# Kernel tuning notes

Hardware: AMD Instinct MI355X
Metric: run time of the kernel (lower is better)

The kernel has to match this reference:

```python
import jax, jax.numpy as jnp
from jax import lax
import numpy as np


def _bn(x, g, b, eps=1e-5):
    # BatchNorm2d in training mode: biased batch stats over (N,H,W) per channel
    m = jnp.mean(x, axis=(0, 2, 3), keepdims=True)
    v = jnp.mean((x - m) ** 2, axis=(0, 2, 3), keepdims=True)
    return (x - m) * lax.rsqrt(v + eps) * g[None, :, None, None] + b[None, :, None, None]


def _conv(x, w, b, pad):
    y = lax.conv_general_dilated(x, w, (1, 1), [(pad, pad), (pad, pad)],
                                 dimension_numbers=('NCHW', 'OIHW', 'NCHW'))
    return y + b[None, :, None, None]


def _prelu(x, a):
    return jnp.where(x >= 0, x, a * x)


def _maxpool2(x):
    return lax.reduce_window(x, -jnp.inf, lax.max, (1, 1, 2, 2), (1, 1, 2, 2), 'VALID')


def _up2(x):
    # UpsamplingBilinear2d(scale_factor=2) -> bilinear, align_corners=True
    B, C, H, W = x.shape
    def idx(n):
        pos = jnp.arange(2 * n, dtype=x.dtype) * (n - 1) / (2 * n - 1)
        lo = jnp.floor(pos).astype(jnp.int32)
        hi = jnp.minimum(lo + 1, n - 1)
        return lo, hi, pos - lo.astype(x.dtype)
    lo, hi, f = idx(H)
    x = x[:, :, lo, :] * (1 - f)[:, None] + x[:, :, hi, :] * f[:, None]
    lo, hi, f = idx(W)
    x = x[:, :, :, lo] * (1 - f) + x[:, :, :, hi] * f
    return x


def _forward(x, n16, sigma16, bias16, prelu_a,
             bn3_g, bn3_b, bn32_g, bn32_b, bn64_g, bn64_b, bn128_g, bn128_b,
             w1, b1, w2, b2, w3, b3, w4, b4, w5, b5, w6, b6, w7, b7, w11, b11):
    B, C, H, W = x.shape
    # 16 enhancement curves fused: r_k = x^{n_k} / (x^{n_k} + sigma_k^{n_k} + bias_k)
    xn = x[None] ** n16[:, None, None, None, None]          # (16,B,3,H,W)
    r = xn / (xn + (sigma16 ** n16)[:, None, None, None, None]
              + bias16[:, None, None, None, None])
    # each branch gets its own BatchNorm2d(3) stats (same affine params)
    r = jax.vmap(lambda t: _bn(t, bn3_g, bn3_b))(r)
    x_fusion = jnp.transpose(r, (1, 0, 2, 3, 4)).reshape(B, 16 * C, H, W)
    x1 = _bn(_maxpool2(_prelu(_conv(x_fusion, w1, b1, 1), prelu_a)), bn32_g, bn32_b)
    x2 = _bn(_maxpool2(_prelu(_conv(x1, w2, b2, 1), prelu_a)), bn64_g, bn64_b)
    x3 = _bn(_maxpool2(_prelu(_conv(x2, w3, b3, 1), prelu_a)), bn128_g, bn128_b)
    x4 = _bn(_conv(x3, w4, b4, 1), bn128_g, bn128_b)
    x5 = _bn(_up2(_prelu(_conv(jnp.concatenate([x4, x3], 1), w5, b5, 1), prelu_a)), bn64_g, bn64_b)
    x6 = _bn(_up2(_prelu(_conv(jnp.concatenate([x2, x5], 1), w6, b6, 1), prelu_a)), bn32_g, bn32_b)
    x_out = jax.nn.sigmoid(_up2(_prelu(_conv(jnp.concatenate([x1, x6], 1), w7, b7, 1), prelu_a)))
    x_out = _conv(x_out, w11, b11, 0)
    x_mean = jnp.mean(x, axis=1, keepdims=True)
    x_out1 = jnp.mean(x_out, axis=1, keepdims=True)
    return x_out1 * (x / (x_mean + 1e-6))


def setup_inputs() -> dict:
    key = jax.random.key(0)
    ks = jax.random.split(key, 16)
    B, H, W = 8, 256, 256
    nf = 32
    x = jax.random.uniform(ks[0], (B, 3, H, W), jnp.float32, 1e-3, 1.0)
    n16 = jnp.arange(1, 17, dtype=jnp.float32) * 0.5
    sigma16 = jnp.full((16,), 0.5, jnp.float32)
    bias16 = jnp.full((16,), 1e-4, jnp.float32)
    prelu_a = jnp.float32(0.25)
    def cw(k, o, i, kk):
        return jax.random.normal(k, (o, i, kk, kk), jnp.float32) * 0.05
    def cb(o):
        return jnp.zeros((o,), jnp.float32)
    return dict(
        x=x, n16=n16, sigma16=sigma16, bias16=bias16, prelu_a=prelu_a,
        bn3_g=jnp.ones((3,), jnp.float32), bn3_b=jnp.zeros((3,), jnp.float32),
        bn32_g=jnp.ones((32,), jnp.float32), bn32_b=jnp.zeros((32,), jnp.float32),
        bn64_g=jnp.ones((64,), jnp.float32), bn64_b=jnp.zeros((64,), jnp.float32),
        bn128_g=jnp.ones((128,), jnp.float32), bn128_b=jnp.zeros((128,), jnp.float32),
        w1=cw(ks[1], nf, 48, 3), b1=cb(nf),
        w2=cw(ks[2], 2 * nf, nf, 3), b2=cb(2 * nf),
        w3=cw(ks[3], 4 * nf, 2 * nf, 3), b3=cb(4 * nf),
        w4=cw(ks[4], 4 * nf, 4 * nf, 3), b4=cb(4 * nf),
        w5=cw(ks[5], 2 * nf, 8 * nf, 3), b5=cb(2 * nf),
        w6=cw(ks[6], nf, 4 * nf, 3), b6=cb(nf),
        w7=cw(ks[7], nf, 2 * nf, 3), b7=cb(nf),
        w11=cw(ks[8], 3, nf, 1), b11=cb(3),
    )


def reference(x, n16, sigma16, bias16, prelu_a,
              bn3_g, bn3_b, bn32_g, bn32_b, bn64_g, bn64_b, bn128_g, bn128_b,
              w1, b1, w2, b2, w3, b3, w4, b4, w5, b5, w6, b6, w7, b7, w11, b11):
    return _forward(x, n16, sigma16, bias16, prelu_a,
                    bn3_g, bn3_b, bn32_g, bn32_b, bn64_g, bn64_b, bn128_g, bn128_b,
                    w1, b1, w2, b2, w3, b3, w4, b4, w5, b5, w6, b6, w7, b7, w11, b11)
```

## Files before the change

### kernel.cpp

```cpp
#include <hip/hip_runtime.h>

#define FAST_EXP2(x) __builtin_amdgcn_exp2f(x)
#define FAST_LOG2(x) __builtin_amdgcn_logf(x)
#define FAST_RCP(x)  __builtin_amdgcn_rcpf(x)

static constexpr size_t S3_SUM=0,   S3_SQ=48;
static constexpr size_t S32A_SUM=96,  S32A_SQ=128;
static constexpr size_t S64A_SUM=160, S64A_SQ=224;
static constexpr size_t S128A_SUM=288,S128A_SQ=416;
static constexpr size_t S128B_SUM=544,S128B_SQ=672;
static constexpr size_t S64B_SUM=800, S64B_SQ=864;
static constexpr size_t S32B_SUM=928, S32B_SQ=960;
static constexpr size_t A3_=1024,  B3_=1072;
static constexpr size_t A32A_=1120, B32A_=1152;
static constexpr size_t A64A_=1184, B64A_=1248;
static constexpr size_t A128A_=1312,B128A_=1440;
static constexpr size_t A128B_=1568,B128B_=1696;
static constexpr size_t A64B_=1824, B64B_=1888;
static constexpr size_t A32B_=1952, B32B_=1984;
static constexpr size_t SPB_=2016, WBAR_=2032, BBAR_=2064;
static constexpr size_t T1_=4096;
static constexpr size_t T2_=T1_+4194304;
static constexpr size_t T3_=T2_+2097152;
static constexpr size_t T4_=T3_+1048576;
static constexpr size_t C5_=T4_+1048576;
static constexpr size_t U5_=C5_+524288;
static constexpr size_t C6_=U5_+2097152;
static constexpr size_t U6_=C6_+1048576;
static constexpr size_t C7_=U6_+4194304;

__global__ void k_precomp(const float* __restrict__ n16, const float* __restrict__ sig16,
                          const float* __restrict__ b16, const float* __restrict__ w11,
                          const float* __restrict__ b11,
                          float* __restrict__ spb, float* __restrict__ wbar, float* __restrict__ bbar)
{
    int t = threadIdx.x;
    if (t < 16) spb[t] = powf(sig16[t], n16[t]) + b16[t];
    else if (t < 48) { int j = t - 16; wbar[j] = (w11[j] + w11[32 + j] + w11[64 + j]) * (1.f/3.f); }
    else if (t == 48) bbar[0] = (b11[0] + b11[1] + b11[2]) * (1.f/3.f);
}

__global__ __launch_bounds__(256) void k_branch_stats(
    const float* __restrict__ x, const float* __restrict__ n16,
    const float* __restrict__ sig16, const float* __restrict__ b16,
    float* __restrict__ sum, float* __restrict__ sq)
{
    const int c = blockIdx.x >> 6;
    const int chunk = blockIdx.x & 63;
    float nk[16], den[16];
#pragma unroll
    for (int k = 0; k < 16; ++k) { nk[k] = n16[k]; den[k] = powf(sig16[k], nk[k]) + b16[k]; }
    float s[16], q[16];
#pragma unroll
    for (int k = 0; k < 16; ++k) { s[k] = 0.f; q[k] = 0.f; }
    const int per = 8192;
    int start = chunk * per;
    for (int i = start + (int)threadIdx.x; i < start + per; i += 256) {
        int b = i >> 16, hw = i & 65535;
        float xv = x[(size_t)(b*3 + c)*65536 + hw];
        float t = FAST_LOG2(xv);
#pragma unroll
        for (int k = 0; k < 16; ++k) {
            float v = FAST_EXP2(nk[k]*t);
            float r = v * FAST_RCP(v + den[k]);
            s[k] += r; q[k] += r*r;
        }
    }
    __shared__ float red[4][32];
    int lane = threadIdx.x & 63, wid = threadIdx.x >> 6;
#pragma unroll
    for (int k = 0; k < 16; ++k) {
#pragma unroll
        for (int off = 32; off > 0; off >>= 1) {
            s[k] += __shfl_down(s[k], off);
            q[k] += __shfl_down(q[k], off);
        }
    }
    if (lane == 0) {
#pragma unroll
        for (int k = 0; k < 16; ++k) { red[wid][k] = s[k]; red[wid][16+k] = q[k]; }
    }
    __syncthreads();
    if (threadIdx.x < 32) {
        float v = red[0][threadIdx.x] + red[1][threadIdx.x] + red[2][threadIdx.x] + red[3][threadIdx.x];
        int k = threadIdx.x & 15;
        if (threadIdx.x < 16) atomicAdd(&sum[k*3 + c], v);
        else                  atomicAdd(&sq[k*3 + c], v);
    }
}

__global__ __launch_bounds__(256) void k_stats(
    const float* __restrict__ in, int C, int HW, int nchunks, int per,
    float* __restrict__ sum, float* __restrict__ sq)
{
    int c = blockIdx.x / nchunks;
    int chunk = blockIdx.x - c*nchunks;
    float s = 0.f, q = 0.f;
    int start = chunk * per, end = start + per;
    for (int i = start + (int)threadIdx.x; i < end; i += 256) {
        int b = i / HW, hw = i - b*HW;
        float v = in[((size_t)b*C + c)*HW + hw];
        s += v; q += v*v;
    }
#pragma unroll
    for (int off = 32; off > 0; off >>= 1) { s += __shfl_down(s, off); q += __shfl_down(q, off); }
    __shared__ float ss[4], qq[4];
    int lane = threadIdx.x & 63, wid = threadIdx.x >> 6;
    if (lane == 0) { ss[wid] = s; qq[wid] = q; }
    __syncthreads();
    if (threadIdx.x == 0) {
        atomicAdd(&sum[c], ss[0]+ss[1]+ss[2]+ss[3]);
        atomicAdd(&sq[c],  qq[0]+qq[1]+qq[2]+qq[3]);
    }
}

__global__ void k_finalize(const float* __restrict__ sum, const float* __restrict__ sq,
                           const float* __restrict__ g, const float* __restrict__ bb,
                           int C, int gdim, float invN,
                           float* __restrict__ A, float* __restrict__ Bs)
{
    int i = blockIdx.x*blockDim.x + threadIdx.x;
    if (i < C) {
        float m   = sum[i]*invN;
        float var = fmaxf(sq[i]*invN - m*m, 0.f);
        float inv = rsqrtf(var + 1e-5f);
        float a   = g[i % gdim]*inv;
        A[i]  = a;
        Bs[i] = bb[i % gdim] - m*a;
    }
}

__global__ __launch_bounds__(256) void k_fill(
    float* __restrict__ out, const float* __restrict__ bias, int C, int HW, int total)
{
    int idx = blockIdx.x*256 + threadIdx.x;
    if (idx < total) {
        int c = (idx / HW) % C;
        out[idx] = bias[c];
    }
}

template<int COG>
__global__ __launch_bounds__(256,3) void k_conv1f(
    const float* __restrict__ x,
    const float* __restrict__ n16, const float* __restrict__ spb,
    const float* __restrict__ A, const float* __restrict__ Bs,
    const float* __restrict__ w, const float* __restrict__ bias,
    const float* __restrict__ prelu_a,
    float* __restrict__ out)
{
    const int tx = threadIdx.x & 15, ty = threadIdx.x >> 4;
    const int nco = 32 / COG;
    const int b = blockIdx.z / nco, cob = (blockIdx.z - b*nco)*COG;
    const int x0 = blockIdx.x*32, y0 = blockIdx.y*32;

    __shared__ float wl[COG*48*9];
    __shared__ float tl[3*1224];
    __shared__ float rl[3*1224];
    __shared__ float al[48], bl[48], nl[16], dl[16];

    for (int t = threadIdx.x; t < COG*48*9; t += 256) {
        int co = t % COG; int rest = t / COG;
        int kk = rest % 9; int ci = rest / 9;
        wl[t] = w[(((size_t)(cob+co))*48 + ci)*9 + kk];
    }
    if (threadIdx.x < 48) { al[threadIdx.x] = A[threadIdx.x]; bl[threadIdx.x] = Bs[threadIdx.x]; }
    else if (threadIdx.x < 64)  nl[threadIdx.x-48] = n16[threadIdx.x-48];
    else if (threadIdx.x < 80)  dl[threadIdx.x-64] = spb[threadIdx.x-64];

    int off_[14]; int chpack = 0; int okf = 0;
#pragma unroll
    for (int j = 0; j < 14; ++j) {
        int i = threadIdx.x + 256*j;
        if (i < 3468) {
            int ch = i / 1156, jj = i - ch*1156;
            int rr = jj / 34, cc = jj - rr*34;
            int gy = y0 - 1 + rr, gx = x0 - 1 + cc;
            bool ok = (unsigned)gy < 256u && (unsigned)gx < 256u;
            off_[j] = ch*1224 + rr*36 + cc;
            chpack |= ch << (2*j);
            if (ok) {
                okf |= 1 << j;
                tl[off_[j]] = FAST_LOG2(x[((size_t)(b*3+ch))*65536 + gy*256 + gx]);
            } else tl[off_[j]] = 0.f;
        } else off_[j] = 3671;
    }

    float acc[COG][4];
#pragma unroll
    for (int i = 0; i < COG; ++i)
#pragma unroll
        for (int j = 0; j < 4; ++j) acc[i][j] = 0.f;

#pragma unroll 1
    for (int k = 0; k < 16; ++k) {
        __syncthreads();
        float nk = nl[k], dk = dl[k];
#pragma unroll
        for (int j = 0; j < 14; ++j) {
            float rv = 0.f;
            if (okf & (1 << j)) {
                int ch = (chpack >> (2*j)) & 3;
                int chg = k*3 + ch;
                float v = FAST_EXP2(nk * tl[off_[j]]);
                rv = v * FAST_RCP(v + dk) * al[chg] + bl[chg];
            }
            rl[off_[j]] = rv;
        }
        __syncthreads();
#pragma unroll
        for (int ch = 0; ch < 3; ++ch) {
            const float* tlp = &rl[ch*1224 + (2*ty)*36 + 2*tx];
            float iv[4][4];
#pragma unroll
            for (int r = 0; r < 4; ++r) {
                float2 a2 = *(const float2*)(tlp + r*36);
                float2 b2 = *(const float2*)(tlp + r*36 + 2);
                iv[r][0]=a2.x; iv[r][1]=a2.y; iv[r][2]=b2.x; iv[r][3]=b2.y;
            }
            const float* wbase = &wl[((k*3+ch)*9)*COG];
#pragma unroll
            for (int kh = 0; kh < 3; ++kh)
#pragma unroll
            for (int kw = 0; kw < 3; ++kw) {
                const int kk = kh*3 + kw;
                float wv[COG];
#pragma unroll
                for (int q = 0; q < COG/4; ++q) {
                    float4 wq = *((const float4*)(wbase + kk*COG) + q);
                    wv[4*q+0]=wq.x; wv[4*q+1]=wq.y; wv[4*q+2]=wq.z; wv[4*q+3]=wq.w;
                }
#pragma unroll
                for (int co = 0; co < COG; ++co)
#pragma unroll
                    for (int py = 0; py < 2; ++py)
#pragma unroll
                        for (int px = 0; px < 2; ++px)
                            acc[co][py*2+px] += wv[co]*iv[py+kh][px+kw];
            }
        }
    }

    float a = __ldg(prelu_a);
    int pyp = (y0 >> 1) + ty, pxp = (x0 >> 1) + tx;
#pragma unroll
    for (int co = 0; co < COG; ++co) {
        float bv = bias[cob + co];
        float v0 = acc[co][0] + bv, v1 = acc[co][1] + bv;
        float v2 = acc[co][2] + bv, v3 = acc[co][3] + bv;
        v0 = v0 >= 0.f ? v0 : a*v0; v1 = v1 >= 0.f ? v1 : a*v1;
        v2 = v2 >= 0.f ? v2 : a*v2; v3 = v3 >= 0.f ? v3 : a*v3;
        out[(((size_t)b*32 + cob + co)*128 + pyp)*128 + pxp] = fmaxf(fmaxf(v0,v1), fmaxf(v2,v3));
    }
}

template<int COG, bool POOL>
__global__ __launch_bounds__(256,4) void k_conv_big(
    const float* __restrict__ in1, int C1,
    const float* __restrict__ sc1, const float* __restrict__ sh1,
    const float* __restrict__ w, const float* __restrict__ bias,
    int Cout, int H, int W, const float* __restrict__ prelu_a, int do_prelu,
    float* __restrict__ out)
{
    const int Cin = C1;
    const int tx = threadIdx.x & 15, ty = threadIdx.x >> 4;
    const int nco = Cout / COG;
    const int b = blockIdx.z / nco, cob = (blockIdx.z - b*nco)*COG;
    const int x0 = blockIdx.x*64, y0 = blockIdx.y*32;

    __shared__ float wl[COG*64*9];
    __shared__ float tile[2][34*68];

    for (int t = threadIdx.x; t < COG*Cin*9; t += 256) {
        int co = t % COG; int rest = t / COG;
        int k = rest % 9; int ci = rest / 9;
        wl[t] = w[(((size_t)(cob+co))*Cin + ci)*9 + k];
    }

    float acc[COG][8];
#pragma unroll
    for (int i = 0; i < COG; ++i)
#pragma unroll
        for (int j = 0; j < 8; ++j) acc[i][j] = 0.f;

#pragma unroll 1
    for (int cb = 0; cb < Cin; cb += 2) {
#pragma unroll
        for (int sub = 0; sub < 2; ++sub) {
            int ci = cb + sub;
            float scv = sc1 ? sc1[ci] : 1.f;
            float shv = sc1 ? sh1[ci] : 0.f;
            const float* base = in1 + ((size_t)b*Cin + ci)*H*W;
#pragma unroll 1
            for (int i = threadIdx.x; i < 34*66; i += 256) {
                int r = i / 66, c = i - r*66;
                int gy = y0 - 1 + r, gx = x0 - 1 + c;
                float v = 0.f;
                if ((unsigned)gy < (unsigned)H && (unsigned)gx < (unsigned)W)
                    v = base[(size_t)gy*W + gx]*scv + shv;
                tile[sub][r*68 + c] = v;
            }
        }
        __syncthreads();
#pragma unroll
        for (int sub = 0; sub < 2; ++sub) {
            const float* tl = &tile[sub][(2*ty)*68 + 4*tx];
            float iv[4][6];
#pragma unroll
            for (int r = 0; r < 4; ++r) {
                float4 av = *(const float4*)(tl + r*68);
                float2 bv = *(const float2*)(tl + r*68 + 4);
                iv[r][0]=av.x; iv[r][1]=av.y; iv[r][2]=av.z; iv[r][3]=av.w;
                iv[r][4]=bv.x; iv[r][5]=bv.y;
            }
            const float* wbase = &wl[(cb+sub)*9*COG];
#pragma unroll
            for (int kh = 0; kh < 3; ++kh)
#pragma unroll
            for (int kw = 0; kw < 3; ++kw) {
                const int k = kh*3 + kw;
                float wv[COG];
#pragma unroll
                for (int q = 0; q < COG/4; ++q) {
                    float4 wq = *((const float4*)(wbase + k*COG) + q);
                    wv[4*q+0]=wq.x; wv[4*q+1]=wq.y; wv[4*q+2]=wq.z; wv[4*q+3]=wq.w;
                }
#pragma unroll
                for (int co = 0; co < COG; ++co)
#pragma unroll
                    for (int py = 0; py < 2; ++py)
#pragma unroll
                        for (int px = 0; px < 4; ++px)
                            acc[co][py*4+px] += wv[co]*iv[py+kh][px+kw];
            }
        }
        __syncthreads();
    }

    float a = __ldg(prelu_a);
    if (POOL) {
        const int Hp = H >> 1, Wp = W >> 1;
        int pyp = (y0 >> 1) + ty, pxp = (x0 >> 1) + 2*tx;
#pragma unroll
        for (int co = 0; co < COG; ++co) {
            float bv = bias[cob + co];
            float v[8];
#pragma unroll
            for (int p = 0; p < 8; ++p) {
                float t = acc[co][p] + bv;
                v[p] = t >= 0.f ? t : a*t;
            }
            float2 st;
            st.x = fmaxf(fmaxf(v[0], v[1]), fmaxf(v[4], v[5]));
            st.y = fmaxf(fmaxf(v[2], v[3]), fmaxf(v[6], v[7]));
            *(float2*)(out + (((size_t)b*Cout + cob + co)*Hp + pyp)*Wp + pxp) = st;
        }
    } else {
        int oy = y0 + 2*ty, ox = x0 + 4*tx;
#pragma unroll
        for (int co = 0; co < COG; ++co) {
            float bv = bias[cob + co];
            float* op = out + (((size_t)b*Cout + cob + co)*H + oy)*W + ox;
#pragma unroll
            for (int py = 0; py < 2; ++py) {
                float4 st;
                float t0 = acc[co][py*4+0] + bv, t1 = acc[co][py*4+1] + bv;
                float t2 = acc[co][py*4+2] + bv, t3 = acc[co][py*4+3] + bv;
                if (do_prelu) {
                    t0 = t0 >= 0.f ? t0 : a*t0; t1 = t1 >= 0.f ? t1 : a*t1;
                    t2 = t2 >= 0.f ? t2 : a*t2; t3 = t3 >= 0.f ? t3 : a*t3;
                }
                st.x=t0; st.y=t1; st.z=t2; st.w=t3;
                *(float4*)(op + py*W) = st;
            }
        }
    }
}

template<int COG, int MAXCI, bool POOL, bool SPLIT>
__global__ __launch_bounds__(256,4) void k_conv32(
    const float* __restrict__ in1, int C1,
    const float* __restrict__ sc1, const float* __restrict__ sh1,
    const float* __restrict__ in2, int C2,
    const float* __restrict__ sc2, const float* __restrict__ sh2,
    const float* __restrict__ w, const float* __restrict__ bias,
    int Cout, int H, int W, const float* __restrict__ prelu_a, int do_prelu,
    int ciN, int nsplit,
    float* __restrict__ out)
{
    const int Cin = C1 + C2;
    const int tx = threadIdx.x & 15, ty = threadIdx.x >> 4;
    const int nco = Cout / COG;
    int z = blockIdx.z;
    const int sp = z % nsplit; z /= nsplit;
    const int b = z / nco, cob = (z - b*nco)*COG;
    const int ci0 = sp * ciN;
    const int x0 = blockIdx.x*32, y0 = blockIdx.y*32;

    __shared__ float wl[COG*MAXCI*9];
    __shared__ float tile[2][34*36];

    for (int t = threadIdx.x; t < COG*ciN*9; t += 256) {
        int co = t % COG; int rest = t / COG;
        int k = rest % 9; int ci = rest / 9;
        wl[t] = w[(((size_t)(cob+co))*Cin + ci0 + ci)*9 + k];
    }

    float acc[COG][4];
#pragma unroll
    for (int i = 0; i < COG; ++i)
#pragma unroll
        for (int j = 0; j < 4; ++j) acc[i][j] = 0.f;

#pragma unroll 1
    for (int cb = 0; cb < ciN; cb += 2) {
#pragma unroll
        for (int sub = 0; sub < 2; ++sub) {
            int ci = ci0 + cb + sub;
            const float* in; int cc; const float* scp; const float* shp; int Cn;
            if (ci < C1) { in = in1; cc = ci;      scp = sc1; shp = sh1; Cn = C1; }
            else         { in = in2; cc = ci - C1; scp = sc2; shp = sh2; Cn = C2; }
            float scv = scp ? scp[cc] : 1.f;
            float shv = scp ? shp[cc] : 0.f;
            const float* base = in + ((size_t)b*Cn + cc)*H*W;
#pragma unroll 1
            for (int i = threadIdx.x; i < 34*34; i += 256) {
                int r = i / 34, c = i - r*34;
                int gy = y0 - 1 + r, gx = x0 - 1 + c;
                float v = 0.f;
                if ((unsigned)gy < (unsigned)H && (unsigned)gx < (unsigned)W)
                    v = base[(size_t)gy*W + gx]*scv + shv;
                tile[sub][r*36 + c] = v;
            }
        }
        __syncthreads();
#pragma unroll
        for (int sub = 0; sub < 2; ++sub) {
            const float* tl = &tile[sub][(2*ty)*36 + 2*tx];
            float iv[4][4];
#pragma unroll
            for (int r = 0; r < 4; ++r) {
                float2 a2 = *(const float2*)(tl + r*36);
                float2 b2 = *(const float2*)(tl + r*36 + 2);
                iv[r][0]=a2.x; iv[r][1]=a2.y; iv[r][2]=b2.x; iv[r][3]=b2.y;
            }
            const float* wbase = &wl[(cb+sub)*9*COG];
#pragma unroll
            for (int kh = 0; kh < 3; ++kh)
#pragma unroll
            for (int kw = 0; kw < 3; ++kw) {
                const int k = kh*3 + kw;
                float wv[COG];
#pragma unroll
                for (int q = 0; q < COG/4; ++q) {
                    float4 wq = *((const float4*)(wbase + k*COG) + q);
                    wv[4*q+0]=wq.x; wv[4*q+1]=wq.y; wv[4*q+2]=wq.z; wv[4*q+3]=wq.w;
                }
#pragma unroll
                for (int co = 0; co < COG; ++co)
#pragma unroll
                    for (int py = 0; py < 2; ++py)
#pragma unroll
                        for (int px = 0; px < 2; ++px)
                            acc[co][py*2+px] += wv[co]*iv[py+kh][px+kw];
            }
        }
        __syncthreads();
    }

    if (SPLIT) {
        int oy = y0 + 2*ty, ox = x0 + 2*tx;
#pragma unroll
        for (int co = 0; co < COG; ++co) {
            float* op = out + (((size_t)b*Cout + cob + co)*H + oy)*W + ox;
            atomicAdd(&op[0],     acc[co][0]);
            atomicAdd(&op[1],     acc[co][1]);
            atomicAdd(&op[W],     acc[co][2]);
            atomicAdd(&op[W + 1], acc[co][3]);
        }
    } else {
        float a = __ldg(prelu_a);
        if (POOL) {
            const int Hp = H >> 1, Wp = W >> 1;
            int pyp = (y0 >> 1) + ty, pxp = (x0 >> 1) + tx;
#pragma unroll
            for (int co = 0; co < COG; ++co) {
                float bv = bias[cob + co];
                float v0 = acc[co][0] + bv, v1 = acc[co][1] + bv;
                float v2 = acc[co][2] + bv, v3 = acc[co][3] + bv;
                v0 = v0 >= 0.f ? v0 : a*v0; v1 = v1 >= 0.f ? v1 : a*v1;
                v2 = v2 >= 0.f ? v2 : a*v2; v3 = v3 >= 0.f ? v3 : a*v3;
                out[(((size_t)b*Cout + cob + co)*Hp + pyp)*Wp + pxp] = fmaxf(fmaxf(v0,v1), fmaxf(v2,v3));
            }
        } else {
            int oy = y0 + 2*ty, ox = x0 + 2*tx;
#pragma unroll
            for (int co = 0; co < COG; ++co) {
                float bv = bias[cob + co];
                float* op = out + (((size_t)b*Cout + cob + co)*H + oy)*W + ox;
                float v0 = acc[co][0] + bv, v1 = acc[co][1] + bv;
                float v2 = acc[co][2] + bv, v3 = acc[co][3] + bv;
                if (do_prelu) {
                    v0 = v0 >= 0.f ? v0 : a*v0; v1 = v1 >= 0.f ? v1 : a*v1;
                    v2 = v2 >= 0.f ? v2 : a*v2; v3 = v3 >= 0.f ? v3 : a*v3;
                }
                op[0] = v0; op[1] = v1; op[W] = v2; op[W+1] = v3;
            }
        }
    }
}

__global__ __launch_bounds__(256) void k_up2(
    const float* __restrict__ in, float* __restrict__ out, int BC, int h, int w,
    const float* __restrict__ prelu_a, int do_prelu)
{
    int idx = blockIdx.x*256 + threadIdx.x;
    int W2 = 2*w, H2 = 2*h;
    int total = BC*H2*W2;
    if (idx >= total) return;
    float a = do_prelu ? __ldg(prelu_a) : 0.f;
    int ox = idx % W2; int t = idx / W2; int oy = t % H2; int bc = t / H2;
    float py = ((float)oy * (float)(h-1)) / (float)(2*h - 1);
    int ly = (int)floorf(py); int hy = min(ly+1, h-1); float fy = py - (float)ly;
    float px = ((float)ox * (float)(w-1)) / (float)(2*w - 1);
    int lx = (int)floorf(px); int hx = min(lx+1, w-1); float fx = px - (float)lx;
    const float* p = in + (size_t)bc*h*w;
    float v00 = p[(size_t)ly*w + lx], v01 = p[(size_t)ly*w + hx];
    float v10 = p[(size_t)hy*w + lx], v11 = p[(size_t)hy*w + hx];
    if (do_prelu) {
        v00 = v00 >= 0.f ? v00 : a*v00;
        v01 = v01 >= 0.f ? v01 : a*v01;
        v10 = v10 >= 0.f ? v10 : a*v10;
        v11 = v11 >= 0.f ? v11 : a*v11;
    }
    float v0 = v00*(1.f-fx) + v01*fx;
    float v1 = v10*(1.f-fx) + v11*fx;
    out[idx] = v0*(1.f-fy) + v1*fy;
}

__global__ __launch_bounds__(256) void k_final(
    const float* __restrict__ c7, const float* __restrict__ x,
    const float* __restrict__ wbar, const float* __restrict__ bbar,
    float* __restrict__ out)
{
    int idx = blockIdx.x*256 + threadIdx.x;
    if (idx >= 8*65536) return;
    int hw = idx & 65535, b = idx >> 16;
    int oy = hw >> 8, ox = hw & 255;
    float py = ((float)oy * 127.f) / 255.f;
    int ly = (int)floorf(py); int hy = min(ly+1, 127); float fy = py - (float)ly;
    float px = ((float)ox * 127.f) / 255.f;
    int lx = (int)floorf(px); int hx = min(lx+1, 127); float fx = px - (float)lx;
    float w00 = (1.f-fy)*(1.f-fx), w01 = (1.f-fy)*fx, w10 = fy*(1.f-fx), w11v = fy*fx;
    const float* base = c7 + (size_t)b*32*16384;
    float accum = bbar[0];
#pragma unroll 8
    for (int j = 0; j < 32; ++j) {
        const float* p = base + (size_t)j*16384;
        float v = p[ly*128 + lx]*w00 + p[ly*128 + hx]*w01 + p[hy*128 + lx]*w10 + p[hy*128 + hx]*w11v;
        float s = FAST_RCP(1.f + __expf(-v));
        accum += wbar[j]*s;
    }
    size_t xb = (size_t)b*3*65536 + hw;
    float x0 = x[xb], x1 = x[xb + 65536], x2 = x[xb + 2*65536];
    float m = (x0 + x1 + x2)*(1.f/3.f) + 1e-6f;
    float sc = accum * FAST_RCP(m);
    out[xb]            = sc*x0;
    out[xb + 65536]    = sc*x1;
    out[xb + 2*65536]  = sc*x2;
}

extern "C" void kernel_launch(void* const* d_in, const int* in_sizes, int n_in,
                              void* d_out, int out_size, void* d_ws, size_t ws_size,
                              hipStream_t stream) {
    const float* x       = (const float*)d_in[0];
    const float* n16     = (const float*)d_in[1];
    const float* sig16   = (const float*)d_in[2];
    const float* bia16   = (const float*)d_in[3];
    const float* prelu_a = (const float*)d_in[4];
    const float* bn3_g   = (const float*)d_in[5];
    const float* bn3_b   = (const float*)d_in[6];
    const float* bn32_g  = (const float*)d_in[7];
    const float* bn32_b  = (const float*)d_in[8];
    const float* bn64_g  = (const float*)d_in[9];
    const float* bn64_b  = (const float*)d_in[10];
    const float* bn128_g = (const float*)d_in[11];
    const float* bn128_b = (const float*)d_in[12];
    const float* w1 = (const float*)d_in[13]; const float* b1 = (const float*)d_in[14];
    const float* w2 = (const float*)d_in[15]; const float* b2 = (const float*)d_in[16];
    const float* w3 = (const float*)d_in[17]; const float* b3 = (const float*)d_in[18];
    const float* w4 = (const float*)d_in[19]; const float* b4 = (const float*)d_in[20];
    const float* w5 = (const float*)d_in[21]; const float* b5 = (const float*)d_in[22];
    const float* w6 = (const float*)d_in[23]; const float* b6 = (const float*)d_in[24];
    const float* w7 = (const float*)d_in[25]; const float* b7 = (const float*)d_in[26];
    const float* w11= (const float*)d_in[27]; const float* b11= (const float*)d_in[28];
    float* ws  = (float*)d_ws;
    float* out = (float*)d_out;

    (void)hipMemsetAsync(d_ws, 0, 4096*sizeof(float), stream);

    k_precomp<<<1, 64, 0, stream>>>(n16, sig16, bia16, w11, b11, ws+SPB_, ws+WBAR_, ws+BBAR_);

    k_branch_stats<<<192, 256, 0, stream>>>(x, n16, sig16, bia16, ws+S3_SUM, ws+S3_SQ);
    k_finalize<<<1, 128, 0, stream>>>(ws+S3_SUM, ws+S3_SQ, bn3_g, bn3_b, 48, 3, 1.f/524288.f, ws+A3_, ws+B3_);

    k_conv1f<8><<<dim3(8,8,32), 256, 0, stream>>>(x, n16, ws+SPB_, ws+A3_, ws+B3_,
                                                  w1, b1, prelu_a, ws+T1_);
    k_stats<<<2048, 256, 0, stream>>>(ws+T1_, 32, 16384, 64, 2048, ws+S32A_SUM, ws+S32A_SQ);
    k_finalize<<<1, 128, 0, stream>>>(ws+S32A_SUM, ws+S32A_SQ, bn32_g, bn32_b, 32, 32, 1.f/131072.f, ws+A32A_, ws+B32A_);

    k_conv_big<8,true><<<dim3(2,4,64), 256, 0, stream>>>(
        ws+T1_, 32, ws+A32A_, ws+B32A_, w2, b2, 64, 128, 128, prelu_a, 1, ws+T2_);
    k_stats<<<1024, 256, 0, stream>>>(ws+T2_, 64, 4096, 16, 2048, ws+S64A_SUM, ws+S64A_SQ);
    k_finalize<<<1, 128, 0, stream>>>(ws+S64A_SUM, ws+S64A_SQ, bn64_g, bn64_b, 64, 64, 1.f/32768.f, ws+A64A_, ws+B64A_);

    k_conv32<8,64,true,false><<<dim3(2,2,128), 256, 0, stream>>>(
        ws+T2_, 64, ws+A64A_, ws+B64A_, nullptr, 0, nullptr, nullptr,
        w3, b3, 128, 64, 64, prelu_a, 1, 64, 1, ws+T3_);
    k_stats<<<512, 256, 0, stream>>>(ws+T3_, 128, 1024, 4, 2048, ws+S128A_SUM, ws+S128A_SQ);
    k_finalize<<<1, 128, 0, stream>>>(ws+S128A_SUM, ws+S128A_SQ, bn128_g, bn128_b, 128, 128, 1.f/8192.f, ws+A128A_, ws+B128A_);

    k_fill<<<4096, 256, 0, stream>>>(ws+T4_, b4, 128, 1024, 1048576);
    k_conv32<8,32,false,true><<<dim3(1,1,512), 256, 0, stream>>>(
        ws+T3_, 128, ws+A128A_, ws+B128A_, nullptr, 0, nullptr, nullptr,
        w4, nullptr, 128, 32, 32, prelu_a, 0, 32, 4, ws+T4_);
    k_stats<<<512, 256, 0, stream>>>(ws+T4_, 128, 1024, 4, 2048, ws+S128B_SUM, ws+S128B_SQ);
    k_finalize<<<1, 128, 0, stream>>>(ws+S128B_SUM, ws+S128B_SQ, bn128_g, bn128_b, 128, 128, 1.f/8192.f, ws+A128B_, ws+B128B_);

    k_fill<<<2048, 256, 0, stream>>>(ws+C5_, b5, 64, 1024, 524288);
    k_conv32<8,32,false,true><<<dim3(1,1,512), 256, 0, stream>>>(
        ws+T4_, 128, ws+A128B_, ws+B128B_, ws+T3_, 128, ws+A128A_, ws+B128A_,
        w5, nullptr, 64, 32, 32, prelu_a, 0, 32, 8, ws+C5_);
    k_up2<<<8192, 256, 0, stream>>>(ws+C5_, ws+U5_, 8*64, 32, 32, prelu_a, 1);
    k_stats<<<1024, 256, 0, stream>>>(ws+U5_, 64, 4096, 16, 2048, ws+S64B_SUM, ws+S64B_SQ);
    k_finalize<<<1, 128, 0, stream>>>(ws+S64B_SUM, ws+S64B_SQ, bn64_g, bn64_b, 64, 64, 1.f/32768.f, ws+A64B_, ws+B64B_);

    k_fill<<<4096, 256, 0, stream>>>(ws+C6_, b6, 32, 4096, 1048576);
    k_conv32<8,32,false,true><<<dim3(2,2,128), 256, 0, stream>>>(
        ws+T2_, 64, ws+A64A_, ws+B64A_, ws+U5_, 64, ws+A64B_, ws+B64B_,
        w6, nullptr, 32, 64, 64, prelu_a, 0, 32, 4, ws+C6_);
    k_up2<<<16384, 256, 0, stream>>>(ws+C6_, ws+U6_, 8*32, 64, 64, prelu_a, 1);
    k_stats<<<2048, 256, 0, stream>>>(ws+U6_, 32, 16384, 64, 2048, ws+S32B_SUM, ws+S32B_SQ);
    k_finalize<<<1, 128, 0, stream>>>(ws+S32B_SUM, ws+S32B_SQ, bn32_g, bn32_b, 32, 32, 1.f/131072.f, ws+A32B_, ws+B32B_);

    k_conv32<8,64,false,false><<<dim3(4,4,32), 256, 0, stream>>>(
        ws+T1_, 32, ws+A32A_, ws+B32A_, ws+U6_, 32, ws+A32B_, ws+B32B_,
        w7, b7, 32, 128, 128, prelu_a, 1, 64, 1, ws+C7_);

    k_final<<<2048, 256, 0, stream>>>(ws+C7_, x, ws+WBAR_, ws+BBAR_, out);
}
```

Measured before the change: 1.447 ms.

## Fuse BatchNorm statistics into conv and upsample epilogues, drop separate stats kernels

```diff
diff --git a/kernel.cpp b/kernel.cpp
--- a/kernel.cpp
+++ b/kernel.cpp
@@ -141,13 +141,39 @@
 }
 
 template<int COG>
-__global__ __launch_bounds__(256,3) void k_conv1f(
+__device__ inline void stats_reduce8(float (&ssum)[COG], float (&ssq)[COG],
+                                     float (*redst)[16], int cob,
+                                     float* __restrict__ gsum, float* __restrict__ gsq)
+{
+    int lane = threadIdx.x & 63, wid = threadIdx.x >> 6;
+#pragma unroll
+    for (int co = 0; co < COG; ++co) {
+#pragma unroll
+        for (int off = 32; off > 0; off >>= 1) {
+            ssum[co] += __shfl_down(ssum[co], off);
+            ssq[co]  += __shfl_down(ssq[co],  off);
+        }
+    }
+    if (lane == 0) {
+#pragma unroll
+        for (int co = 0; co < COG; ++co) { redst[wid][co] = ssum[co]; redst[wid][8+co] = ssq[co]; }
+    }
+    __syncthreads();
+    if (threadIdx.x < 16) {
+        float v = redst[0][threadIdx.x] + redst[1][threadIdx.x] + redst[2][threadIdx.x] + redst[3][threadIdx.x];
+        if (threadIdx.x < 8) atomicAdd(&gsum[cob + threadIdx.x], v);
+        else                 atomicAdd(&gsq[cob + threadIdx.x - 8], v);
+    }
+}
+
+template<int COG>
+__global__ __launch_bounds__(256,4) void k_conv1f(
     const float* __restrict__ x,
     const float* __restrict__ n16, const float* __restrict__ spb,
     const float* __restrict__ A, const float* __restrict__ Bs,
     const float* __restrict__ w, const float* __restrict__ bias,
     const float* __restrict__ prelu_a,
-    float* __restrict__ out)
+    float* __restrict__ out, float* __restrict__ gsum, float* __restrict__ gsq)
 {
     const int tx = threadIdx.x & 15, ty = threadIdx.x >> 4;
     const int nco = 32 / COG;
@@ -155,9 +181,9 @@
     const int x0 = blockIdx.x*32, y0 = blockIdx.y*32;
 
     __shared__ float wl[COG*48*9];
-    __shared__ float tl[3*1224];
     __shared__ float rl[3*1224];
     __shared__ float al[48], bl[48], nl[16], dl[16];
+    __shared__ float redst[4][16];
 
     for (int t = threadIdx.x; t < COG*48*9; t += 256) {
         int co = t % COG; int rest = t / COG;
@@ -168,6 +194,7 @@
     else if (threadIdx.x < 64)  nl[threadIdx.x-48] = n16[threadIdx.x-48];
     else if (threadIdx.x < 80)  dl[threadIdx.x-64] = spb[threadIdx.x-64];
 
+    float tlr[14];
     int off_[14]; int chpack = 0; int okf = 0;
 #pragma unroll
     for (int j = 0; j < 14; ++j) {
@@ -179,11 +206,12 @@
             bool ok = (unsigned)gy < 256u && (unsigned)gx < 256u;
             off_[j] = ch*1224 + rr*36 + cc;
             chpack |= ch << (2*j);
+            tlr[j] = 0.f;
             if (ok) {
                 okf |= 1 << j;
-                tl[off_[j]] = FAST_LOG2(x[((size_t)(b*3+ch))*65536 + gy*256 + gx]);
-            } else tl[off_[j]] = 0.f;
-        } else off_[j] = 3671;
+                tlr[j] = FAST_LOG2(x[((size_t)(b*3+ch))*65536 + gy*256 + gx]);
+            }
+        } else { off_[j] = 3671; tlr[j] = 0.f; }
     }
 
     float acc[COG][4];
@@ -202,7 +230,7 @@
             if (okf & (1 << j)) {
                 int ch = (chpack >> (2*j)) & 3;
                 int chg = k*3 + ch;
-                float v = FAST_EXP2(nk * tl[off_[j]]);
+                float v = FAST_EXP2(nk * tlr[j]);
                 rv = v * FAST_RCP(v + dk) * al[chg] + bl[chg];
             }
             rl[off_[j]] = rv;
@@ -243,6 +271,7 @@
 
     float a = __ldg(prelu_a);
     int pyp = (y0 >> 1) + ty, pxp = (x0 >> 1) + tx;
+    float ssum[COG], ssq[COG];
 #pragma unroll
     for (int co = 0; co < COG; ++co) {
         float bv = bias[cob + co];
@@ -250,8 +279,12 @@
         float v2 = acc[co][2] + bv, v3 = acc[co][3] + bv;
         v0 = v0 >= 0.f ? v0 : a*v0; v1 = v1 >= 0.f ? v1 : a*v1;
         v2 = v2 >= 0.f ? v2 : a*v2; v3 = v3 >= 0.f ? v3 : a*v3;
-        out[(((size_t)b*32 + cob + co)*128 + pyp)*128 + pxp] = fmaxf(fmaxf(v0,v1), fmaxf(v2,v3));
-    }
+        float m = fmaxf(fmaxf(v0,v1), fmaxf(v2,v3));
+        out[(((size_t)b*32 + cob + co)*128 + pyp)*128 + pxp] = m;
+        ssum[co] = m; ssq[co] = m*m;
+    }
+    __syncthreads();
+    stats_reduce8<COG>(ssum, ssq, redst, cob, gsum, gsq);
 }
 
 template<int COG, bool POOL>
@@ -260,7 +293,7 @@
     const float* __restrict__ sc1, const float* __restrict__ sh1,
     const float* __restrict__ w, const float* __restrict__ bias,
     int Cout, int H, int W, const float* __restrict__ prelu_a, int do_prelu,
-    float* __restrict__ out)
+    float* __restrict__ out, float* __restrict__ gsum, float* __restrict__ gsq)
 {
     const int Cin = C1;
     const int tx = threadIdx.x & 15, ty = threadIdx.x >> 4;
@@ -270,6 +303,7 @@
 
     __shared__ float wl[COG*64*9];
     __shared__ float tile[2][34*68];
+    __shared__ float redst[4][16];
 
     for (int t = threadIdx.x; t < COG*Cin*9; t += 256) {
         int co = t % COG; int rest = t / COG;
@@ -338,6 +372,7 @@
     }
 
     float a = __ldg(prelu_a);
+    float ssum[COG], ssq[COG];
     if (POOL) {
         const int Hp = H >> 1, Wp = W >> 1;
         int pyp = (y0 >> 1) + ty, pxp = (x0 >> 1) + 2*tx;
@@ -354,7 +389,9 @@
             st.x = fmaxf(fmaxf(v[0], v[1]), fmaxf(v[4], v[5]));
             st.y = fmaxf(fmaxf(v[2], v[3]), fmaxf(v[6], v[7]));
             *(float2*)(out + (((size_t)b*Cout + cob + co)*Hp + pyp)*Wp + pxp) = st;
-        }
+            ssum[co] = st.x + st.y; ssq[co] = st.x*st.x + st.y*st.y;
+        }
+        stats_reduce8<COG>(ssum, ssq, redst, cob, gsum, gsq);
     } else {
         int oy = y0 + 2*ty, ox = x0 + 4*tx;
 #pragma unroll
@@ -377,7 +414,7 @@
     }
 }
 
-template<int COG, int MAXCI, bool POOL, bool SPLIT>
+template<int COG, int MAXCI, bool POOL, bool SPLIT, bool STATS>
 __global__ __launch_bounds__(256,4) void k_conv32(
     const float* __restrict__ in1, int C1,
     const float* __restrict__ sc1, const float* __restrict__ sh1,
@@ -386,7 +423,7 @@
     const float* __restrict__ w, const float* __restrict__ bias,
     int Cout, int H, int W, const float* __restrict__ prelu_a, int do_prelu,
     int ciN, int nsplit,
-    float* __restrict__ out)
+    float* __restrict__ out, float* __restrict__ gsum, float* __restrict__ gsq)
 {
     const int Cin = C1 + C2;
     const int tx = threadIdx.x & 15, ty = threadIdx.x >> 4;
@@ -399,6 +436,7 @@
 
     __shared__ float wl[COG*MAXCI*9];
     __shared__ float tile[2][34*36];
+    __shared__ float redst[4][16];
 
     for (int t = threadIdx.x; t < COG*ciN*9; t += 256) {
         int co = t % COG; int rest = t / COG;
@@ -480,6 +518,7 @@
         }
     } else {
         float a = __ldg(prelu_a);
+        float ssum[COG], ssq[COG];
         if (POOL) {
             const int Hp = H >> 1, Wp = W >> 1;
             int pyp = (y0 >> 1) + ty, pxp = (x0 >> 1) + tx;
@@ -490,8 +529,11 @@
                 float v2 = acc[co][2] + bv, v3 = acc[co][3] + bv;
                 v0 = v0 >= 0.f ? v0 : a*v0; v1 = v1 >= 0.f ? v1 : a*v1;
                 v2 = v2 >= 0.f ? v2 : a*v2; v3 = v3 >= 0.f ? v3 : a*v3;
-                out[(((size_t)b*Cout + cob + co)*Hp + pyp)*Wp + pxp] = fmaxf(fmaxf(v0,v1), fmaxf(v2,v3));
-            }
+                float m = fmaxf(fmaxf(v0,v1), fmaxf(v2,v3));
+                out[(((size_t)b*Cout + cob + co)*Hp + pyp)*Wp + pxp] = m;
+                ssum[co] = m; ssq[co] = m*m;
+            }
+            if (STATS) stats_reduce8<COG>(ssum, ssq, redst, cob, gsum, gsq);
         } else {
             int oy = y0 + 2*ty, ox = x0 + 2*tx;
 #pragma unroll
@@ -505,19 +547,20 @@
                     v2 = v2 >= 0.f ? v2 : a*v2; v3 = v3 >= 0.f ? v3 : a*v3;
                 }
                 op[0] = v0; op[1] = v1; op[W] = v2; op[W+1] = v3;
-            }
+                ssum[co] = v0+v1+v2+v3; ssq[co] = v0*v0+v1*v1+v2*v2+v3*v3;
+            }
+            if (STATS) stats_reduce8<COG>(ssum, ssq, redst, cob, gsum, gsq);
         }
     }
 }
 
 __global__ __launch_bounds__(256) void k_up2(
-    const float* __restrict__ in, float* __restrict__ out, int BC, int h, int w,
-    const float* __restrict__ prelu_a, int do_prelu)
+    const float* __restrict__ in, float* __restrict__ out, int C, int h, int w,
+    const float* __restrict__ prelu_a, int do_prelu,
+    float* __restrict__ gsum, float* __restrict__ gsq)
 {
     int idx = blockIdx.x*256 + threadIdx.x;
     int W2 = 2*w, H2 = 2*h;
-    int total = BC*H2*W2;
-    if (idx >= total) return;
     float a = do_prelu ? __ldg(prelu_a) : 0.f;
     int ox = idx % W2; int t = idx / W2; int oy = t % H2; int bc = t / H2;
     float py = ((float)oy * (float)(h-1)) / (float)(2*h - 1);
@@ -535,7 +578,20 @@
     }
     float v0 = v00*(1.f-fx) + v01*fx;
     float v1 = v10*(1.f-fx) + v11*fx;
-    out[idx] = v0*(1.f-fy) + v1*fy;
+    float v = v0*(1.f-fy) + v1*fy;
+    out[idx] = v;
+    float s = v, q = v*v;
+#pragma unroll
+    for (int off = 32; off > 0; off >>= 1) { s += __shfl_down(s, off); q += __shfl_down(q, off); }
+    __shared__ float ss[4], qq[4];
+    int lane = threadIdx.x & 63, wid = threadIdx.x >> 6;
+    if (lane == 0) { ss[wid] = s; qq[wid] = q; }
+    __syncthreads();
+    if (threadIdx.x == 0) {
+        int c = bc % C;
+        atomicAdd(&gsum[c], ss[0]+ss[1]+ss[2]+ss[3]);
+        atomicAdd(&gsq[c],  qq[0]+qq[1]+qq[2]+qq[3]);
+    }
 }
 
 __global__ __launch_bounds__(256) void k_final(
@@ -605,47 +661,43 @@
     k_finalize<<<1, 128, 0, stream>>>(ws+S3_SUM, ws+S3_SQ, bn3_g, bn3_b, 48, 3, 1.f/524288.f, ws+A3_, ws+B3_);
 
     k_conv1f<8><<<dim3(8,8,32), 256, 0, stream>>>(x, n16, ws+SPB_, ws+A3_, ws+B3_,
-                                                  w1, b1, prelu_a, ws+T1_);
-    k_stats<<<2048, 256, 0, stream>>>(ws+T1_, 32, 16384, 64, 2048, ws+S32A_SUM, ws+S32A_SQ);
+                                                  w1, b1, prelu_a, ws+T1_, ws+S32A_SUM, ws+S32A_SQ);
     k_finalize<<<1, 128, 0, stream>>>(ws+S32A_SUM, ws+S32A_SQ, bn32_g, bn32_b, 32, 32, 1.f/131072.f, ws+A32A_, ws+B32A_);
 
     k_conv_big<8,true><<<dim3(2,4,64), 256, 0, stream>>>(
-        ws+T1_, 32, ws+A32A_, ws+B32A_, w2, b2, 64, 128, 128, prelu_a, 1, ws+T2_);
-    k_stats<<<1024, 256, 0, stream>>>(ws+T2_, 64, 4096, 16, 2048, ws+S64A_SUM, ws+S64A_SQ);
+        ws+T1_, 32, ws+A32A_, ws+B32A_, w2, b2, 64, 128, 128, prelu_a, 1,
+        ws+T2_, ws+S64A_SUM, ws+S64A_SQ);
     k_finalize<<<1, 128, 0, stream>>>(ws+S64A_SUM, ws+S64A_SQ, bn64_g, bn64_b, 64, 64, 1.f/32768.f, ws+A64A_, ws+B64A_);
 
-    k_conv32<8,64,true,false><<<dim3(2,2,128), 256, 0, stream>>>(
+    k_conv32<8,64,true,false,true><<<dim3(2,2,128), 256, 0, stream>>>(
         ws+T2_, 64, ws+A64A_, ws+B64A_, nullptr, 0, nullptr, nullptr,
-        w3, b3, 128, 64, 64, prelu_a, 1, 64, 1, ws+T3_);
-    k_stats<<<512, 256, 0, stream>>>(ws+T3_, 128, 1024, 4, 2048, ws+S128A_SUM, ws+S128A_SQ);
+        w3, b3, 128, 64, 64, prelu_a, 1, 64, 1, ws+T3_, ws+S128A_SUM, ws+S128A_SQ);
     k_finalize<<<1, 128, 0, stream>>>(ws+S128A_SUM, ws+S128A_SQ, bn128_g, bn128_b, 128, 128, 1.f/8192.f, ws+A128A_, ws+B128A_);
 
     k_fill<<<4096, 256, 0, stream>>>(ws+T4_, b4, 128, 1024, 1048576);
-    k_conv32<8,32,false,true><<<dim3(1,1,512), 256, 0, stream>>>(
+    k_conv32<8,32,false,true,false><<<dim3(1,1,512), 256, 0, stream>>>(
         ws+T3_, 128, ws+A128A_, ws+B128A_, nullptr, 0, nullptr, nullptr,
-        w4, nullptr, 128, 32, 32, prelu_a, 0, 32, 4, ws+T4_);
+        w4, nullptr, 128, 32, 32, prelu_a, 0, 32, 4, ws+T4_, nullptr, nullptr);
     k_stats<<<512, 256, 0, stream>>>(ws+T4_, 128, 1024, 4, 2048, ws+S128B_SUM, ws+S128B_SQ);
     k_finalize<<<1, 128, 0, stream>>>(ws+S128B_SUM, ws+S128B_SQ, bn128_g, bn128_b, 128, 128, 1.f/8192.f, ws+A128B_, ws+B128B_);
 
     k_fill<<<2048, 256, 0, stream>>>(ws+C5_, b5, 64, 1024, 524288);
-    k_conv32<8,32,false,true><<<dim3(1,1,512), 256, 0, stream>>>(
+    k_conv32<8,32,false,true,false><<<dim3(1,1,512), 256, 0, stream>>>(
         ws+T4_, 128, ws+A128B_, ws+B128B_, ws+T3_, 128, ws+A128A_, ws+B128A_,
-        w5, nullptr, 64, 32, 32, prelu_a, 0, 32, 8, ws+C5_);
-    k_up2<<<8192, 256, 0, stream>>>(ws+C5_, ws+U5_, 8*64, 32, 32, prelu_a, 1);
-    k_stats<<<1024, 256, 0, stream>>>(ws+U5_, 64, 4096, 16, 2048, ws+S64B_SUM, ws+S64B_SQ);
+        w5, nullptr, 64, 32, 32, prelu_a, 0, 32, 8, ws+C5_, nullptr, nullptr);
+    k_up2<<<8192, 256, 0, stream>>>(ws+C5_, ws+U5_, 64, 32, 32, prelu_a, 1, ws+S64B_SUM, ws+S64B_SQ);
     k_finalize<<<1, 128, 0, stream>>>(ws+S64B_SUM, ws+S64B_SQ, bn64_g, bn64_b, 64, 64, 1.f/32768.f, ws+A64B_, ws+B64B_);
 
     k_fill<<<4096, 256, 0, stream>>>(ws+C6_, b6, 32, 4096, 1048576);
-    k_conv32<8,32,false,true><<<dim3(2,2,128), 256, 0, stream>>>(
+    k_conv32<8,32,false,true,false><<<dim3(2,2,128), 256, 0, stream>>>(
         ws+T2_, 64, ws+A64A_, ws+B64A_, ws+U5_, 64, ws+A64B_, ws+B64B_,
-        w6, nullptr, 32, 64, 64, prelu_a, 0, 32, 4, ws+C6_);
-    k_up2<<<16384, 256, 0, stream>>>(ws+C6_, ws+U6_, 8*32, 64, 64, prelu_a, 1);
-    k_stats<<<2048, 256, 0, stream>>>(ws+U6_, 32, 16384, 64, 2048, ws+S32B_SUM, ws+S32B_SQ);
+        w6, nullptr, 32, 64, 64, prelu_a, 0, 32, 4, ws+C6_, nullptr, nullptr);
+    k_up2<<<16384, 256, 0, stream>>>(ws+C6_, ws+U6_, 32, 64, 64, prelu_a, 1, ws+S32B_SUM, ws+S32B_SQ);
     k_finalize<<<1, 128, 0, stream>>>(ws+S32B_SUM, ws+S32B_SQ, bn32_g, bn32_b, 32, 32, 1.f/131072.f, ws+A32B_, ws+B32B_);
 
-    k_conv32<8,64,false,false><<<dim3(4,4,32), 256, 0, stream>>>(
+    k_conv32<8,64,false,false,false><<<dim3(4,4,32), 256, 0, stream>>>(
         ws+T1_, 32, ws+A32A_, ws+B32A_, ws+U6_, 32, ws+A32B_, ws+B32B_,
-        w7, b7, 32, 128, 128, prelu_a, 1, 64, 1, ws+C7_);
+        w7, b7, 32, 128, 128, prelu_a, 1, 64, 1, ws+C7_, nullptr, nullptr);
 
     k_final<<<2048, 256, 0, stream>>>(ws+C7_, x, ws+WBAR_, ws+BBAR_, out);
 }
```

New measurement: 1.521 ms. +5.1%, slower.
